# Kernel tuning notes

Measured on AMD Instinct MI355X. Metric: run time of the kernel, lower is better.

## Reference

```python
import jax, jax.numpy as jnp
import numpy as np

N_NODES = 100000


def gcn_conv(h, W, b, src, dst, n):
    # h: [N, Fin] -> [N, Fout], GCNConv with symmetric normalization + self-loops
    h = h @ W  # transform first (PyG order): [N, Fout]
    loop = jnp.arange(n, dtype=src.dtype)
    src_sl = jnp.concatenate([src, loop])  # [E+N]
    dst_sl = jnp.concatenate([dst, loop])
    deg = jax.ops.segment_sum(jnp.ones_like(dst_sl, dtype=h.dtype), dst_sl, num_segments=n)  # [N]
    dinv = jax.lax.rsqrt(deg)  # deg >= 1 thanks to self-loops
    norm = dinv[src_sl] * dinv[dst_sl]  # [E+N]
    msgs = h[src_sl] * norm[:, None]  # gather + scale: [E+N, Fout]
    out = jax.ops.segment_sum(msgs, dst_sl, num_segments=n)  # scatter-add
    return out + b


def setup_inputs() -> dict:
    key = jax.random.key(0)
    kx, ke, k1, k2 = jax.random.split(key, 4)
    in_dim, hid_dim, out_dim = 512, 128, 40
    x = jax.random.normal(kx, (N_NODES, in_dim), dtype=jnp.float32)
    edge_index = jax.random.randint(ke, (2, 1600000), 0, N_NODES, dtype=jnp.int64)
    s1 = 1.0 / np.sqrt(in_dim)
    s2 = 1.0 / np.sqrt(hid_dim)
    W1 = jax.random.uniform(k1, (in_dim, hid_dim), jnp.float32, -s1, s1)
    b1 = jnp.zeros((hid_dim,), jnp.float32)
    W2 = jax.random.uniform(k2, (hid_dim, out_dim), jnp.float32, -s2, s2)
    b2 = jnp.zeros((out_dim,), jnp.float32)
    return {"x": x, "edge_index": edge_index, "W1": W1, "b1": b1, "W2": W2, "b2": b2}


def reference(x, edge_index, W1, b1, W2, b2):
    src, dst = edge_index[0], edge_index[1]
    n = x.shape[0]
    h = jax.nn.relu(gcn_conv(x, W1, b1, src, dst, n))
    h = gcn_conv(h, W2, b2, src, dst, n)
    return jax.nn.log_softmax(h, axis=1)
```

## Files before the change

### kernel.cpp

```cpp
#include <hip/hip_runtime.h>
#include <math.h>

#define FIN 512
#define FH 128
#define FOUT 40
#define FP 64
#define NB 512
#define PSLOTS 30
#define CAPG 4096
#define PBLK 512

typedef unsigned char u8;
typedef __attribute__((ext_vector_type(8))) short bf16x8;
typedef __attribute__((ext_vector_type(4))) float f32x4;
typedef __attribute__((ext_vector_type(2))) float f32x2;

__device__ inline ushort f2bf(float f){
  union { float f; uint32_t u; } v; v.f = f;
  uint32_t u = v.u;
  uint32_t r = (u + 0x7FFF + ((u >> 16) & 1)) >> 16;
  return (ushort)r;
}
__device__ inline uint32_t cvtpk(float a, float b){
  uint32_t r;
  asm("v_cvt_pk_bf16_f32 %0, %1, %2" : "=v"(r) : "v"(a), "v"(b));
  return r;
}
__device__ inline f32x2 pkadd(f32x2 a, f32x2 b){
  f32x2 r;
  asm("v_pk_add_f32 %0, %1, %2" : "=v"(r) : "v"(a), "v"(b));
  return r;
}
__device__ inline f32x2 f8lo(uint32_t v){ return __builtin_amdgcn_cvt_pk_f32_fp8(v, false); }
__device__ inline f32x2 f8hi(uint32_t v){ return __builtin_amdgcn_cvt_pk_f32_fp8(v, true); }
__device__ inline u8 f2f8(float v){
  return (u8)(__builtin_amdgcn_cvt_pk_fp8_f32(v, v, 0, false) & 0xFF);
}

__global__ __launch_bounds__(256) void k_part(const int* __restrict__ src,
                                              const int* __restrict__ dst, int e,
                                              int* __restrict__ gcur,
                                              uint32_t* __restrict__ gbuf, int n, int npb,
                                              const float* __restrict__ W1,
                                              const float* __restrict__ W2,
                                              ushort* __restrict__ W1t, ushort* __restrict__ W2t){
  __shared__ uint32_t pbuf[NB*PSLOTS];
  __shared__ int lcnt[NB];
  int b = blockIdx.x, t = threadIdx.x;
  int gidx = b*256 + t;
  if(gidx < FIN*FH){
    int k = gidx / FH, c = gidx % FH;
    W1t[(size_t)c*FIN + k] = f2bf(W1[gidx]);
  }
  if(gidx < 48*FH){
    int c = gidx / FH, k = gidx % FH;
    W2t[gidx] = (c < FOUT) ? f2bf(W2[(size_t)k*FOUT + c]) : (ushort)0;
  }
  for(int i=t;i<NB;i+=256) lcnt[i]=0;
  __syncthreads();
  int chunk = (e + PBLK - 1) / PBLK;
  int base = b * chunk;
  int endE = base + chunk; if(endE > e) endE = e;
  if(base >= e) return;
  int rounds = (endE - base + 255) / 256;
  for(int rr=0; rr<rounds; ++rr){
    int i = base + rr*256 + t;
    if(i < endE){
      int s = src[i];
      int d = dst[i];
      int bk = d / npb;
      uint32_t pk_ = ((uint32_t)s << 8) | (uint32_t)(d - bk*npb);
      int slot = atomicAdd(&lcnt[bk], 1);
      if(slot < PSLOTS){
        pbuf[bk*PSLOTS + slot] = pk_;
      } else {
        int g = atomicAdd(&gcur[bk], 1);
        gbuf[(size_t)bk*CAPG + g] = pk_;
      }
    }
    __syncthreads();
    bool last = (rr == rounds-1);
    for(int tb=t; tb<NB; tb+=256){
      int c = lcnt[tb];
      int k = c < PSLOTS ? c : PSLOTS;
      if(k > 0 && (k >= 16 || last)){
        int g = atomicAdd(&gcur[tb], k);
        uint32_t* dstp = &gbuf[(size_t)tb*CAPG + g];
        const uint32_t* srcp = &pbuf[tb*PSLOTS];
        for(int q=0; q<k; q++) dstp[q] = srcp[q];
        lcnt[tb] = 0;
      }
    }
    __syncthreads();
  }
}

__global__ __launch_bounds__(512) void k_scan_g(const int* __restrict__ gcur,
                                                int* __restrict__ bstart){
  __shared__ int sh[512];
  int t = threadIdx.x;
  sh[t] = gcur[t];
  __syncthreads();
  for(int off=1; off<512; off<<=1){
    int x = (t>=off)? sh[t-off]:0; __syncthreads();
    sh[t]+=x; __syncthreads();
  }
  bstart[t] = (t>0)? sh[t-1] : 0;
}

__global__ __launch_bounds__(256) void k_histfill(const uint32_t* __restrict__ gbuf,
                                                  const int* __restrict__ gcur,
                                                  const int* __restrict__ bstart,
                                                  int* __restrict__ rp, float* __restrict__ dinv,
                                                  int* __restrict__ srcs, int n, int npb){
  __shared__ int hist[256];
  __shared__ int sh[256];
  __shared__ int lcur[256];
  int b = blockIdx.x, t = threadIdx.x;
  int base = b * npb;
  if(base >= n) return;
  int nn = n - base; if(nn > npb) nn = npb;
  hist[t] = 0;
  __syncthreads();
  int m = gcur[b];
  const uint32_t* bp = gbuf + (size_t)b*CAPG;
  for(int i=t; i<m; i+=256) atomicAdd(&hist[bp[i] & 255u], 1);
  __syncthreads();
  int v = hist[t];
  sh[t] = v;
  __syncthreads();
  for(int off=1; off<256; off<<=1){
    int x = (t>=off)? sh[t-off]:0; __syncthreads();
    sh[t]+=x; __syncthreads();
  }
  int bs = bstart[b];
  if(t < nn){
    rp[base+t+1] = bs + sh[t];
    dinv[base+t] = rsqrtf((float)(v+1));
    lcur[t] = bs + sh[t] - v;
  }
  if(b==0 && t==0) rp[0] = 0;
  __syncthreads();
  for(int i=t; i<m; i+=256){
    uint32_t w = bp[i];
    int ld = (int)(w & 255u);
    int p = atomicAdd(&lcur[ld], 1);
    srcs[p] = (int)(w >> 8);
  }
}

__global__ __launch_bounds__(512, 2) void k_gemm1(const float* __restrict__ X,
                                                  const ushort* __restrict__ W1t,
                                                  const float* __restrict__ dinv,
                                                  u8* __restrict__ XWs, int n){
  __shared__ char smem[32768];
  int t = threadIdx.x;
  int gi = blockIdx.x;
  int lane = t & 63;
  int wid = t >> 6;
  int l15 = lane & 15;
  int lk8 = (lane >> 4) * 8;
  int rowbase = gi * 256 + wid * 32;

  int r0 = rowbase + l15;      if (r0 >= n) r0 = n-1;
  int r1 = rowbase + 16 + l15; if (r1 >= n) r1 = n-1;
  const float* a0p = X + (size_t)r0*FIN;
  const float* a1p = X + (size_t)r1*FIN;

  f32x4 acc[2][8];
  #pragma unroll
  for(int i=0;i<2;i++)
    #pragma unroll
    for(int j=0;j<8;j++) acc[i][j] = (f32x4){0.f,0.f,0.f,0.f};

  char* WsB = smem;

  for(int ph=0; ph<4; ph++){
    if(ph) __syncthreads();
    #pragma unroll
    for(int it=0; it<4; it++){
      int c = it*512 + t;
      int col = c >> 4, kslot = c & 15;
      uint4 v = *(const uint4*)(W1t + (size_t)col*FIN + ph*128 + kslot*8);
      int dstb = col*256 + ((kslot*16) ^ ((col & 7) << 4));
      *(uint4*)(WsB + dstb) = v;
    }
    __syncthreads();

    for(int kc=0; kc<4; kc++){
      int kl = kc*32 + lk8;
      int kg = ph*128 + kl;
      float4 a0a = *(const float4*)(a0p + kg);
      float4 a0b = *(const float4*)(a0p + kg + 4);
      float4 a1a = *(const float4*)(a1p + kg);
      float4 a1b = *(const float4*)(a1p + kg + 4);
      uint4 fa0u, fa1u;
      fa0u.x = cvtpk(a0a.x, a0a.y); fa0u.y = cvtpk(a0a.z, a0a.w);
      fa0u.z = cvtpk(a0b.x, a0b.y); fa0u.w = cvtpk(a0b.z, a0b.w);
      fa1u.x = cvtpk(a1a.x, a1a.y); fa1u.y = cvtpk(a1a.z, a1a.w);
      fa1u.z = cvtpk(a1b.x, a1b.y); fa1u.w = cvtpk(a1b.z, a1b.w);
      bf16x8 fa0 = *(bf16x8*)&fa0u;
      bf16x8 fa1 = *(bf16x8*)&fa1u;

      #pragma unroll
      for(int fj=0; fj<8; fj++){
        int col = fj*16 + l15;
        int srcb = col*256 + ((kl*2) ^ ((col & 7) << 4));
        bf16x8 fb = *(const bf16x8*)(WsB + srcb);
        acc[0][fj] = __builtin_amdgcn_mfma_f32_16x16x32_bf16(fa0, fb, acc[0][fj], 0, 0, 0);
        acc[1][fj] = __builtin_amdgcn_mfma_f32_16x16x32_bf16(fa1, fb, acc[1][fj], 0, 0, 0);
      }
    }
  }

  int rbase = (lane >> 4) * 4;
  #pragma unroll
  for(int fi=0; fi<2; fi++){
    #pragma unroll
    for(int r=0; r<4; r++){
      int row = rowbase + fi*16 + rbase + r;
      if(row < n){
        float dd = dinv[row];
        #pragma unroll
        for(int fj=0; fj<8; fj++){
          XWs[(size_t)row*FH + fj*16 + l15] = f2f8(acc[fi][fj][r] * dd);
        }
      }
    }
  }
}

__global__ __launch_bounds__(256) void k_agg1(const u8* __restrict__ XWs, const int* __restrict__ rp,
                                              const int* __restrict__ srcs, const float* __restrict__ dinv,
                                              const float* __restrict__ b1, ushort* __restrict__ H1b, int n){
  int d = blockIdx.x*4 + (threadIdx.x >> 6);
  if(d >= n) return;
  int lane = threadIdx.x & 63;
  int g = lane >> 3, li = lane & 7;
  f32x2 acc[8];
  #pragma unroll
  for(int k=0;k<8;k++) acc[k] = (f32x2){0.f,0.f};
  int beg = rp[d];
  int end = rp[d+1];
  int j = beg + g;
  bool h0 = j < end, h1 = j + 8 < end;
  int s0 = 0, s1 = 0;
  if(h0) s0 = srcs[j];
  if(h1) s1 = srcs[j+8];
  while(h1){
    int nj = j + 16;
    bool nh0 = nj < end, nh1 = nj + 8 < end;
    int ns0 = 0, ns1 = 0;
    if(nh0) ns0 = srcs[nj];
    if(nh1) ns1 = srcs[nj+8];
    uint4 a0 = *(const uint4*)(XWs + (size_t)s0*FH + li*16);
    uint4 c0 = *(const uint4*)(XWs + (size_t)s1*FH + li*16);
    acc[0] = pkadd(acc[0], pkadd(f8lo(a0.x), f8lo(c0.x)));
    acc[1] = pkadd(acc[1], pkadd(f8hi(a0.x), f8hi(c0.x)));
    acc[2] = pkadd(acc[2], pkadd(f8lo(a0.y), f8lo(c0.y)));
    acc[3] = pkadd(acc[3], pkadd(f8hi(a0.y), f8hi(c0.y)));
    acc[4] = pkadd(acc[4], pkadd(f8lo(a0.z), f8lo(c0.z)));
    acc[5] = pkadd(acc[5], pkadd(f8hi(a0.z), f8hi(c0.z)));
    acc[6] = pkadd(acc[6], pkadd(f8lo(a0.w), f8lo(c0.w)));
    acc[7] = pkadd(acc[7], pkadd(f8hi(a0.w), f8hi(c0.w)));
    j = nj; s0 = ns0; s1 = ns1; h0 = nh0; h1 = nh1;
  }
  if(h0){
    uint4 a0 = *(const uint4*)(XWs + (size_t)s0*FH + li*16);
    acc[0] = pkadd(acc[0], f8lo(a0.x));
    acc[1] = pkadd(acc[1], f8hi(a0.x));
    acc[2] = pkadd(acc[2], f8lo(a0.y));
    acc[3] = pkadd(acc[3], f8hi(a0.y));
    acc[4] = pkadd(acc[4], f8lo(a0.z));
    acc[5] = pkadd(acc[5], f8hi(a0.z));
    acc[6] = pkadd(acc[6], f8lo(a0.w));
    acc[7] = pkadd(acc[7], f8hi(a0.w));
  }
  #pragma unroll
  for(int k=0;k<8;k++){
    #pragma unroll
    for(int c=0;c<2;c++){
      acc[k][c] += __shfl_xor(acc[k][c], 8);
      acc[k][c] += __shfl_xor(acc[k][c], 16);
      acc[k][c] += __shfl_xor(acc[k][c], 32);
    }
  }
  if(g == 0){
    uint4 sv4 = *(const uint4*)(XWs + (size_t)d*FH + li*16);
    f32x2 slf[8];
    slf[0]=f8lo(sv4.x); slf[1]=f8hi(sv4.x); slf[2]=f8lo(sv4.y); slf[3]=f8hi(sv4.y);
    slf[4]=f8lo(sv4.z); slf[5]=f8hi(sv4.z); slf[6]=f8lo(sv4.w); slf[7]=f8hi(sv4.w);
    float dd = dinv[d];
    uint32_t w[8];
    #pragma unroll
    for(int k=0;k<8;k++){
      float b0 = b1[li*16 + k*2];
      float b1v = b1[li*16 + k*2 + 1];
      float o0 = fmaxf((acc[k][0]+slf[k][0])*dd + b0, 0.f);
      float o1 = fmaxf((acc[k][1]+slf[k][1])*dd + b1v, 0.f);
      w[k] = cvtpk(o0, o1);
    }
    uint4 w0 = {w[0],w[1],w[2],w[3]};
    uint4 w1 = {w[4],w[5],w[6],w[7]};
    uint4* wp = (uint4*)(H1b + (size_t)d*FH + li*16);
    wp[0] = w0;
    wp[1] = w1;
  }
}

__global__ __launch_bounds__(256) void k_gemm2_mfma(const ushort* __restrict__ H1b,
                                                    const ushort* __restrict__ W2t,
                                                    const float* __restrict__ dinv,
                                                    u8* __restrict__ H2s, int n){
  int t = threadIdx.x;
  int lane = t & 63;
  int wid = t >> 6;
  int l15 = lane & 15;
  int lk8 = (lane >> 4) * 8;
  int rowbase = blockIdx.x * 128 + wid * 32;

  int r0 = rowbase + l15;      if (r0 >= n) r0 = n-1;
  int r1 = rowbase + 16 + l15; if (r1 >= n) r1 = n-1;
  const ushort* a0p = H1b + (size_t)r0*FH + lk8;
  const ushort* a1p = H1b + (size_t)r1*FH + lk8;

  f32x4 acc[2][3];
  #pragma unroll
  for(int i=0;i<2;i++)
    #pragma unroll
    for(int j=0;j<3;j++) acc[i][j] = (f32x4){0.f,0.f,0.f,0.f};

  #pragma unroll
  for(int kc=0; kc<4; kc++){
    int k0 = kc*32;
    bf16x8 fa0 = *(const bf16x8*)(a0p + k0);
    bf16x8 fa1 = *(const bf16x8*)(a1p + k0);
    #pragma unroll
    for(int fj=0; fj<3; fj++){
      bf16x8 fb = *(const bf16x8*)(W2t + (size_t)(fj*16 + l15)*FH + k0 + lk8);
      acc[0][fj] = __builtin_amdgcn_mfma_f32_16x16x32_bf16(fa0, fb, acc[0][fj], 0, 0, 0);
      acc[1][fj] = __builtin_amdgcn_mfma_f32_16x16x32_bf16(fa1, fb, acc[1][fj], 0, 0, 0);
    }
  }

  int rbase = (lane >> 4) * 4;
  #pragma unroll
  for(int fi=0; fi<2; fi++){
    #pragma unroll
    for(int r=0; r<4; r++){
      int row = rowbase + fi*16 + rbase + r;
      if(row < n){
        float dd = dinv[row];
        #pragma unroll
        for(int fj=0; fj<3; fj++){
          int col = fj*16 + l15;
          H2s[(size_t)row*FP + col] = (col < FOUT) ? f2f8(acc[fi][fj][r] * dd) : (u8)0;
        }
        H2s[(size_t)row*FP + 48 + l15] = (u8)0;
      }
    }
  }
}

__global__ __launch_bounds__(256) void k_agg2_sm(const u8* __restrict__ H2s, const int* __restrict__ rp,
                                                 const int* __restrict__ srcs, const float* __restrict__ dinv,
                                                 const float* __restrict__ b2, float* __restrict__ out, int n){
  int d = blockIdx.x*4 + (threadIdx.x >> 6);
  if(d >= n) return;
  int lane = threadIdx.x & 63;
  int g = lane >> 3, li = lane & 7;
  f32x2 acc[4];
  #pragma unroll
  for(int k=0;k<4;k++) acc[k] = (f32x2){0.f,0.f};
  int beg = rp[d];
  int end = rp[d+1];
  int j = beg + g;
  bool h0 = j < end, h1 = j + 8 < end;
  int s0 = 0, s1 = 0;
  if(h0) s0 = srcs[j];
  if(h1) s1 = srcs[j+8];
  while(h1){
    int nj = j + 16;
    bool nh0 = nj < end, nh1 = nj + 8 < end;
    int ns0 = 0, ns1 = 0;
    if(nh0) ns0 = srcs[nj];
    if(nh1) ns1 = srcs[nj+8];
    uint2 v = *(const uint2*)(H2s + (size_t)s0*FP + li*8);
    uint2 u = *(const uint2*)(H2s + (size_t)s1*FP + li*8);
    acc[0] = pkadd(acc[0], pkadd(f8lo(v.x), f8lo(u.x)));
    acc[1] = pkadd(acc[1], pkadd(f8hi(v.x), f8hi(u.x)));
    acc[2] = pkadd(acc[2], pkadd(f8lo(v.y), f8lo(u.y)));
    acc[3] = pkadd(acc[3], pkadd(f8hi(v.y), f8hi(u.y)));
    j = nj; s0 = ns0; s1 = ns1; h0 = nh0; h1 = nh1;
  }
  if(h0){
    uint2 v = *(const uint2*)(H2s + (size_t)s0*FP + li*8);
    acc[0] = pkadd(acc[0], f8lo(v.x));
    acc[1] = pkadd(acc[1], f8hi(v.x));
    acc[2] = pkadd(acc[2], f8lo(v.y));
    acc[3] = pkadd(acc[3], f8hi(v.y));
  }
  #pragma unroll
  for(int k=0;k<4;k++){
    #pragma unroll
    for(int c=0;c<2;c++){
      acc[k][c] += __shfl_xor(acc[k][c], 8);
      acc[k][c] += __shfl_xor(acc[k][c], 16);
      acc[k][c] += __shfl_xor(acc[k][c], 32);
    }
  }
  uint2 sv = *(const uint2*)(H2s + (size_t)d*FP + li*8);
  f32x2 s2[4] = { f8lo(sv.x), f8hi(sv.x), f8lo(sv.y), f8hi(sv.y) };
  float dd = dinv[d];
  float val[8];
  #pragma unroll
  for(int k=0;k<4;k++){
    #pragma unroll
    for(int c=0;c<2;c++){
      int col = li*8 + k*2 + c;
      float bv = (col < FOUT) ? b2[col] : 0.f;
      val[k*2+c] = (col < FOUT) ? ((acc[k][c]+s2[k][c])*dd + bv) : -3.402823466e38f;
    }
  }
  float m = val[0];
  #pragma unroll
  for(int k=1;k<8;k++) m = fmaxf(m, val[k]);
  #pragma unroll
  for(int off=1; off<8; off<<=1) m = fmaxf(m, __shfl_xor(m, off));
  float ssum = 0.f;
  #pragma unroll
  for(int k=0;k<8;k++){
    int col = li*8 + k;
    ssum += (col < FOUT) ? expf(val[k] - m) : 0.f;
  }
  #pragma unroll
  for(int off=1; off<8; off<<=1) ssum += __shfl_xor(ssum, off);
  float lse = m + logf(ssum);
  if(g == 0 && li < 5){
    float4 o0 = {val[0]-lse, val[1]-lse, val[2]-lse, val[3]-lse};
    float4 o1 = {val[4]-lse, val[5]-lse, val[6]-lse, val[7]-lse};
    float* op = out + (size_t)d*FOUT + li*8;
    *(float4*)op = o0;
    *(float4*)(op+4) = o1;
  }
}


extern "C" void kernel_launch(void* const* d_in, const int* in_sizes, int n_in,
                              void* d_out, int out_size, void* d_ws, size_t ws_size,
                              hipStream_t stream){
  const float* X  = (const float*)d_in[0];
  const int*   ei = (const int*)d_in[1];
  const float* W1 = (const float*)d_in[2];
  const float* b1 = (const float*)d_in[3];
  const float* W2 = (const float*)d_in[4];
  const float* b2 = (const float*)d_in[5];
  float* out = (float*)d_out;

  int n = in_sizes[0] / FIN;
  int e = in_sizes[1] / 2;
  const int* src = ei;
  const int* dst = ei + e;

  int npb = (n + NB - 1) / NB;

  u8* XWs     = (u8*)d_ws;
  ushort* H1b = (ushort*)(XWs + (size_t)n*FH);
  u8* H2s     = (u8*)(H1b + (size_t)n*FH);
  ushort* W1t = (ushort*)(H2s + (size_t)n*FP);
  ushort* W2t = W1t + (size_t)FH*FIN;
  float* dinv = (float*)(W2t + 48*FH);
  int* gcur   = (int*)(dinv + n);
  int* bstart = gcur + NB;
  int* rp     = bstart + NB;
  int* srcs   = rp + (n+1) + 3;
  uint32_t* gbuf = (uint32_t*)H1b;

  int G = (n + 255) / 256;

  hipMemsetAsync(gcur, 0, (size_t)NB*sizeof(int), stream);
  hipLaunchKernelGGL(k_part, dim3(PBLK), dim3(256), 0, stream,
                     src, dst, e, gcur, gbuf, n, npb, W1, W2, W1t, W2t);
  hipLaunchKernelGGL(k_scan_g, dim3(1), dim3(512), 0, stream, gcur, bstart);
  hipLaunchKernelGGL(k_histfill, dim3(NB), dim3(256), 0, stream,
                     gbuf, gcur, bstart, rp, dinv, srcs, n, npb);

  hipLaunchKernelGGL(k_gemm1, dim3(G), dim3(512), 0, stream, X, W1t, dinv, XWs, n);

  hipLaunchKernelGGL(k_agg1, dim3((n+3)/4), dim3(256), 0, stream, XWs, rp, srcs, dinv, b1, H1b, n);
  hipLaunchKernelGGL(k_gemm2_mfma, dim3((n+127)/128), dim3(256), 0, stream, H1b, W2t, dinv, H2s, n);
  hipLaunchKernelGGL(k_agg2_sm, dim3((n+3)/4), dim3(256), 0, stream, H2s, rp, srcs, dinv, b2, out, n);
}
```

Measured before the change: 239.1 us.

## Fuse edge partitioning with GEMM1 in one launch by interleaving block roles

Edge partitioning and the first GEMM now run in one kernel, with odd blocks doing the partition and even blocks doing the GEMM, so the memory-bound partition overlaps the MFMA work. Because the GEMM now runs before the degree/dinv computation, the source-side dinv scaling moves out of the GEMM epilogue into agg1, which gathers dinv[src] per edge and uses packed FMAs. Weight conversion is split into its own small prep kernel. The cost is one extra dinv gather per edge in the aggregation and higher shared-memory use per block, which may lower occupancy.

```diff
diff --git a/kernel.cpp b/kernel.cpp
--- a/kernel.cpp
+++ b/kernel.cpp
@@ -31,67 +31,159 @@
   asm("v_pk_add_f32 %0, %1, %2" : "=v"(r) : "v"(a), "v"(b));
   return r;
 }
+__device__ inline f32x2 pkfma(f32x2 a, f32x2 b, f32x2 c){
+  f32x2 r;
+  asm("v_pk_fma_f32 %0, %1, %2, %3" : "=v"(r) : "v"(a), "v"(b), "v"(c));
+  return r;
+}
 __device__ inline f32x2 f8lo(uint32_t v){ return __builtin_amdgcn_cvt_pk_f32_fp8(v, false); }
 __device__ inline f32x2 f8hi(uint32_t v){ return __builtin_amdgcn_cvt_pk_f32_fp8(v, true); }
 __device__ inline u8 f2f8(float v){
   return (u8)(__builtin_amdgcn_cvt_pk_fp8_f32(v, v, 0, false) & 0xFF);
 }
 
-__global__ __launch_bounds__(256) void k_part(const int* __restrict__ src,
-                                              const int* __restrict__ dst, int e,
-                                              int* __restrict__ gcur,
-                                              uint32_t* __restrict__ gbuf, int n, int npb,
-                                              const float* __restrict__ W1,
+__global__ __launch_bounds__(256) void k_prep(const float* __restrict__ W1,
                                               const float* __restrict__ W2,
                                               ushort* __restrict__ W1t, ushort* __restrict__ W2t){
-  __shared__ uint32_t pbuf[NB*PSLOTS];
-  __shared__ int lcnt[NB];
-  int b = blockIdx.x, t = threadIdx.x;
-  int gidx = b*256 + t;
-  if(gidx < FIN*FH){
-    int k = gidx / FH, c = gidx % FH;
-    W1t[(size_t)c*FIN + k] = f2bf(W1[gidx]);
-  }
-  if(gidx < 48*FH){
-    int c = gidx / FH, k = gidx % FH;
-    W2t[gidx] = (c < FOUT) ? f2bf(W2[(size_t)k*FOUT + c]) : (ushort)0;
-  }
-  for(int i=t;i<NB;i+=256) lcnt[i]=0;
-  __syncthreads();
-  int chunk = (e + PBLK - 1) / PBLK;
-  int base = b * chunk;
-  int endE = base + chunk; if(endE > e) endE = e;
-  if(base >= e) return;
-  int rounds = (endE - base + 255) / 256;
-  for(int rr=0; rr<rounds; ++rr){
-    int i = base + rr*256 + t;
-    if(i < endE){
-      int s = src[i];
-      int d = dst[i];
-      int bk = d / npb;
-      uint32_t pk_ = ((uint32_t)s << 8) | (uint32_t)(d - bk*npb);
-      int slot = atomicAdd(&lcnt[bk], 1);
-      if(slot < PSLOTS){
-        pbuf[bk*PSLOTS + slot] = pk_;
-      } else {
-        int g = atomicAdd(&gcur[bk], 1);
-        gbuf[(size_t)bk*CAPG + g] = pk_;
+  int i = blockIdx.x*256 + threadIdx.x;
+  if(i < FIN*FH){
+    int k = i / FH, c = i % FH;
+    W1t[(size_t)c*FIN + k] = f2bf(W1[i]);
+  }
+  if(i < 48*FH){
+    int c = i / FH, k = i % FH;
+    W2t[i] = (c < FOUT) ? f2bf(W2[(size_t)k*FOUT + c]) : (ushort)0;
+  }
+}
+
+__global__ __launch_bounds__(512, 2) void k_gemm1_part(const float* __restrict__ X,
+                                                       const ushort* __restrict__ W1t,
+                                                       u8* __restrict__ XWs, int n, int G,
+                                                       const int* __restrict__ src,
+                                                       const int* __restrict__ dst, int e,
+                                                       int* __restrict__ gcur,
+                                                       uint32_t* __restrict__ gbuf, int npb){
+  __shared__ char smem[63488];
+  int b = blockIdx.x;
+  int t = threadIdx.x;
+
+  if(b & 1){
+    int pidx = b >> 1;
+    if(pidx >= PBLK) return;
+    uint32_t* pbuf = (uint32_t*)smem;
+    int* lcnt = (int*)(smem + NB*PSLOTS*4);
+    if(t < NB) lcnt[t] = 0;
+    __syncthreads();
+    int chunk = (e + PBLK - 1) / PBLK;
+    int base = pidx * chunk;
+    int endE = base + chunk; if(endE > e) endE = e;
+    if(base >= e) return;
+    int rounds = (endE - base + 511) / 512;
+    for(int rr=0; rr<rounds; ++rr){
+      int i = base + rr*512 + t;
+      if(i < endE){
+        int s = src[i];
+        int d = dst[i];
+        int bk = d / npb;
+        uint32_t pk_ = ((uint32_t)s << 8) | (uint32_t)(d - bk*npb);
+        int slot = atomicAdd(&lcnt[bk], 1);
+        if(slot < PSLOTS){
+          pbuf[bk*PSLOTS + slot] = pk_;
+        } else {
+          int g = atomicAdd(&gcur[bk], 1);
+          gbuf[(size_t)bk*CAPG + g] = pk_;
+        }
       }
+      __syncthreads();
+      bool last = (rr == rounds-1);
+      if(t < NB){
+        int c = lcnt[t];
+        int k = c < PSLOTS ? c : PSLOTS;
+        if(k > 0 && (k >= 16 || last)){
+          int g = atomicAdd(&gcur[t], k);
+          uint32_t* dstp = &gbuf[(size_t)t*CAPG + g];
+          const uint32_t* srcp = &pbuf[t*PSLOTS];
+          for(int q=0; q<k; q++) dstp[q] = srcp[q];
+          lcnt[t] = 0;
+        }
+      }
+      __syncthreads();
+    }
+    return;
+  }
+
+  int gi = b >> 1;
+  if(gi >= G) return;
+  int lane = t & 63;
+  int wid = t >> 6;
+  int l15 = lane & 15;
+  int lk8 = (lane >> 4) * 8;
+  int rowbase = gi * 256 + wid * 32;
+
+  int r0 = rowbase + l15;      if (r0 >= n) r0 = n-1;
+  int r1 = rowbase + 16 + l15; if (r1 >= n) r1 = n-1;
+  const float* a0p = X + (size_t)r0*FIN;
+  const float* a1p = X + (size_t)r1*FIN;
+
+  f32x4 acc[2][8];
+  #pragma unroll
+  for(int i=0;i<2;i++)
+    #pragma unroll
+    for(int j=0;j<8;j++) acc[i][j] = (f32x4){0.f,0.f,0.f,0.f};
+
+  char* WsB = smem;
+
+  for(int ph=0; ph<4; ph++){
+    if(ph) __syncthreads();
+    #pragma unroll
+    for(int it=0; it<4; it++){
+      int c = it*512 + t;
+      int col = c >> 4, kslot = c & 15;
+      uint4 v = *(const uint4*)(W1t + (size_t)col*FIN + ph*128 + kslot*8);
+      int dstb = col*256 + ((kslot*16) ^ ((col & 7) << 4));
+      *(uint4*)(WsB + dstb) = v;
     }
     __syncthreads();
-    bool last = (rr == rounds-1);
-    for(int tb=t; tb<NB; tb+=256){
-      int c = lcnt[tb];
-      int k = c < PSLOTS ? c : PSLOTS;
-      if(k > 0 && (k >= 16 || last)){
-        int g = atomicAdd(&gcur[tb], k);
-        uint32_t* dstp = &gbuf[(size_t)tb*CAPG + g];
-        const uint32_t* srcp = &pbuf[tb*PSLOTS];
-        for(int q=0; q<k; q++) dstp[q] = srcp[q];
-        lcnt[tb] = 0;
+
+    for(int kc=0; kc<4; kc++){
+      int kl = kc*32 + lk8;
+      int kg = ph*128 + kl;
+      float4 a0a = *(const float4*)(a0p + kg);
+      float4 a0b = *(const float4*)(a0p + kg + 4);
+      float4 a1a = *(const float4*)(a1p + kg);
+      float4 a1b = *(const float4*)(a1p + kg + 4);
+      uint4 fa0u, fa1u;
+      fa0u.x = cvtpk(a0a.x, a0a.y); fa0u.y = cvtpk(a0a.z, a0a.w);
+      fa0u.z = cvtpk(a0b.x, a0b.y); fa0u.w = cvtpk(a0b.z, a0b.w);
+      fa1u.x = cvtpk(a1a.x, a1a.y); fa1u.y = cvtpk(a1a.z, a1a.w);
+      fa1u.z = cvtpk(a1b.x, a1b.y); fa1u.w = cvtpk(a1b.z, a1b.w);
+      bf16x8 fa0 = *(bf16x8*)&fa0u;
+      bf16x8 fa1 = *(bf16x8*)&fa1u;
+
+      #pragma unroll
+      for(int fj=0; fj<8; fj++){
+        int col = fj*16 + l15;
+        int srcb = col*256 + ((kl*2) ^ ((col & 7) << 4));
+        bf16x8 fb = *(const bf16x8*)(WsB + srcb);
+        acc[0][fj] = __builtin_amdgcn_mfma_f32_16x16x32_bf16(fa0, fb, acc[0][fj], 0, 0, 0);
+        acc[1][fj] = __builtin_amdgcn_mfma_f32_16x16x32_bf16(fa1, fb, acc[1][fj], 0, 0, 0);
       }
     }
-    __syncthreads();
+  }
+
+  int rbase = (lane >> 4) * 4;
+  #pragma unroll
+  for(int fi=0; fi<2; fi++){
+    #pragma unroll
+    for(int r=0; r<4; r++){
+      int row = rowbase + fi*16 + rbase + r;
+      if(row < n){
+        #pragma unroll
+        for(int fj=0; fj<8; fj++){
+          XWs[(size_t)row*FH + fj*16 + l15] = f2f8(acc[fi][fj][r]);
+        }
+      }
+    }
   }
 }
 
@@ -149,87 +241,6 @@
   }
 }
 
-__global__ __launch_bounds__(512, 2) void k_gemm1(const float* __restrict__ X,
-                                                  const ushort* __restrict__ W1t,
-                                                  const float* __restrict__ dinv,
-                                                  u8* __restrict__ XWs, int n){
-  __shared__ char smem[32768];
-  int t = threadIdx.x;
-  int gi = blockIdx.x;
-  int lane = t & 63;
-  int wid = t >> 6;
-  int l15 = lane & 15;
-  int lk8 = (lane >> 4) * 8;
-  int rowbase = gi * 256 + wid * 32;
-
-  int r0 = rowbase + l15;      if (r0 >= n) r0 = n-1;
-  int r1 = rowbase + 16 + l15; if (r1 >= n) r1 = n-1;
-  const float* a0p = X + (size_t)r0*FIN;
-  const float* a1p = X + (size_t)r1*FIN;
-
-  f32x4 acc[2][8];
-  #pragma unroll
-  for(int i=0;i<2;i++)
-    #pragma unroll
-    for(int j=0;j<8;j++) acc[i][j] = (f32x4){0.f,0.f,0.f,0.f};
-
-  char* WsB = smem;
-
-  for(int ph=0; ph<4; ph++){
-    if(ph) __syncthreads();
-    #pragma unroll
-    for(int it=0; it<4; it++){
-      int c = it*512 + t;
-      int col = c >> 4, kslot = c & 15;
-      uint4 v = *(const uint4*)(W1t + (size_t)col*FIN + ph*128 + kslot*8);
-      int dstb = col*256 + ((kslot*16) ^ ((col & 7) << 4));
-      *(uint4*)(WsB + dstb) = v;
-    }
-    __syncthreads();
-
-    for(int kc=0; kc<4; kc++){
-      int kl = kc*32 + lk8;
-      int kg = ph*128 + kl;
-      float4 a0a = *(const float4*)(a0p + kg);
-      float4 a0b = *(const float4*)(a0p + kg + 4);
-      float4 a1a = *(const float4*)(a1p + kg);
-      float4 a1b = *(const float4*)(a1p + kg + 4);
-      uint4 fa0u, fa1u;
-      fa0u.x = cvtpk(a0a.x, a0a.y); fa0u.y = cvtpk(a0a.z, a0a.w);
-      fa0u.z = cvtpk(a0b.x, a0b.y); fa0u.w = cvtpk(a0b.z, a0b.w);
-      fa1u.x = cvtpk(a1a.x, a1a.y); fa1u.y = cvtpk(a1a.z, a1a.w);
-      fa1u.z = cvtpk(a1b.x, a1b.y); fa1u.w = cvtpk(a1b.z, a1b.w);
-      bf16x8 fa0 = *(bf16x8*)&fa0u;
-      bf16x8 fa1 = *(bf16x8*)&fa1u;
-
-      #pragma unroll
-      for(int fj=0; fj<8; fj++){
-        int col = fj*16 + l15;
-        int srcb = col*256 + ((kl*2) ^ ((col & 7) << 4));
-        bf16x8 fb = *(const bf16x8*)(WsB + srcb);
-        acc[0][fj] = __builtin_amdgcn_mfma_f32_16x16x32_bf16(fa0, fb, acc[0][fj], 0, 0, 0);
-        acc[1][fj] = __builtin_amdgcn_mfma_f32_16x16x32_bf16(fa1, fb, acc[1][fj], 0, 0, 0);
-      }
-    }
-  }
-
-  int rbase = (lane >> 4) * 4;
-  #pragma unroll
-  for(int fi=0; fi<2; fi++){
-    #pragma unroll
-    for(int r=0; r<4; r++){
-      int row = rowbase + fi*16 + rbase + r;
-      if(row < n){
-        float dd = dinv[row];
-        #pragma unroll
-        for(int fj=0; fj<8; fj++){
-          XWs[(size_t)row*FH + fj*16 + l15] = f2f8(acc[fi][fj][r] * dd);
-        }
-      }
-    }
-  }
-}
-
 __global__ __launch_bounds__(256) void k_agg1(const u8* __restrict__ XWs, const int* __restrict__ rp,
                                               const int* __restrict__ srcs, const float* __restrict__ dinv,
                                               const float* __restrict__ b1, ushort* __restrict__ H1b, int n){
@@ -245,36 +256,41 @@
   int j = beg + g;
   bool h0 = j < end, h1 = j + 8 < end;
   int s0 = 0, s1 = 0;
-  if(h0) s0 = srcs[j];
-  if(h1) s1 = srcs[j+8];
+  float ds0 = 0.f, ds1 = 0.f;
+  if(h0){ s0 = srcs[j];   ds0 = dinv[s0]; }
+  if(h1){ s1 = srcs[j+8]; ds1 = dinv[s1]; }
   while(h1){
     int nj = j + 16;
     bool nh0 = nj < end, nh1 = nj + 8 < end;
     int ns0 = 0, ns1 = 0;
-    if(nh0) ns0 = srcs[nj];
-    if(nh1) ns1 = srcs[nj+8];
+    float nds0 = 0.f, nds1 = 0.f;
+    if(nh0){ ns0 = srcs[nj];   nds0 = dinv[ns0]; }
+    if(nh1){ ns1 = srcs[nj+8]; nds1 = dinv[ns1]; }
     uint4 a0 = *(const uint4*)(XWs + (size_t)s0*FH + li*16);
     uint4 c0 = *(const uint4*)(XWs + (size_t)s1*FH + li*16);
-    acc[0] = pkadd(acc[0], pkadd(f8lo(a0.x), f8lo(c0.x)));
-    acc[1] = pkadd(acc[1], pkadd(f8hi(a0.x), f8hi(c0.x)));
-    acc[2] = pkadd(acc[2], pkadd(f8lo(a0.y), f8lo(c0.y)));
-    acc[3] = pkadd(acc[3], pkadd(f8hi(a0.y), f8hi(c0.y)));
-    acc[4] = pkadd(acc[4], pkadd(f8lo(a0.z), f8lo(c0.z)));
-    acc[5] = pkadd(acc[5], pkadd(f8hi(a0.z), f8hi(c0.z)));
-    acc[6] = pkadd(acc[6], pkadd(f8lo(a0.w), f8lo(c0.w)));
-    acc[7] = pkadd(acc[7], pkadd(f8hi(a0.w), f8hi(c0.w)));
-    j = nj; s0 = ns0; s1 = ns1; h0 = nh0; h1 = nh1;
+    f32x2 d0v = {ds0, ds0};
+    f32x2 d1v = {ds1, ds1};
+    acc[0] = pkfma(f8lo(a0.x), d0v, acc[0]); acc[0] = pkfma(f8lo(c0.x), d1v, acc[0]);
+    acc[1] = pkfma(f8hi(a0.x), d0v, acc[1]); acc[1] = pkfma(f8hi(c0.x), d1v, acc[1]);
+    acc[2] = pkfma(f8lo(a0.y), d0v, acc[2]); acc[2] = pkfma(f8lo(c0.y), d1v, acc[2]);
+    acc[3] = pkfma(f8hi(a0.y), d0v, acc[3]); acc[3] = pkfma(f8hi(c0.y), d1v, acc[3]);
+    acc[4] = pkfma(f8lo(a0.z), d0v, acc[4]); acc[4] = pkfma(f8lo(c0.z), d1v, acc[4]);
+    acc[5] = pkfma(f8hi(a0.z), d0v, acc[5]); acc[5] = pkfma(f8hi(c0.z), d1v, acc[5]);
+    acc[6] = pkfma(f8lo(a0.w), d0v, acc[6]); acc[6] = pkfma(f8lo(c0.w), d1v, acc[6]);
+    acc[7] = pkfma(f8hi(a0.w), d0v, acc[7]); acc[7] = pkfma(f8hi(c0.w), d1v, acc[7]);
+    j = nj; s0 = ns0; s1 = ns1; ds0 = nds0; ds1 = nds1; h0 = nh0; h1 = nh1;
   }
   if(h0){
     uint4 a0 = *(const uint4*)(XWs + (size_t)s0*FH + li*16);
-    acc[0] = pkadd(acc[0], f8lo(a0.x));
-    acc[1] = pkadd(acc[1], f8hi(a0.x));
-    acc[2] = pkadd(acc[2], f8lo(a0.y));
-    acc[3] = pkadd(acc[3], f8hi(a0.y));
-    acc[4] = pkadd(acc[4], f8lo(a0.z));
-    acc[5] = pkadd(acc[5], f8hi(a0.z));
-    acc[6] = pkadd(acc[6], f8lo(a0.w));
-    acc[7] = pkadd(acc[7], f8hi(a0.w));
+    f32x2 d0v = {ds0, ds0};
+    acc[0] = pkfma(f8lo(a0.x), d0v, acc[0]);
+    acc[1] = pkfma(f8hi(a0.x), d0v, acc[1]);
+    acc[2] = pkfma(f8lo(a0.y), d0v, acc[2]);
+    acc[3] = pkfma(f8hi(a0.y), d0v, acc[3]);
+    acc[4] = pkfma(f8lo(a0.z), d0v, acc[4]);
+    acc[5] = pkfma(f8hi(a0.z), d0v, acc[5]);
+    acc[6] = pkfma(f8lo(a0.w), d0v, acc[6]);
+    acc[7] = pkfma(f8hi(a0.w), d0v, acc[7]);
   }
   #pragma unroll
   for(int k=0;k<8;k++){
@@ -296,8 +312,8 @@
     for(int k=0;k<8;k++){
       float b0 = b1[li*16 + k*2];
       float b1v = b1[li*16 + k*2 + 1];
-      float o0 = fmaxf((acc[k][0]+slf[k][0])*dd + b0, 0.f);
-      float o1 = fmaxf((acc[k][1]+slf[k][1])*dd + b1v, 0.f);
+      float o0 = fmaxf((acc[k][0] + slf[k][0]*dd)*dd + b0, 0.f);
+      float o1 = fmaxf((acc[k][1] + slf[k][1]*dd)*dd + b1v, 0.f);
       w[k] = cvtpk(o0, o1);
     }
     uint4 w0 = {w[0],w[1],w[2],w[3]};
@@ -477,16 +493,16 @@
   uint32_t* gbuf = (uint32_t*)H1b;
 
   int G = (n + 255) / 256;
+  int T = 2 * ((G > PBLK) ? G : PBLK);
 
   hipMemsetAsync(gcur, 0, (size_t)NB*sizeof(int), stream);
-  hipLaunchKernelGGL(k_part, dim3(PBLK), dim3(256), 0, stream,
-                     src, dst, e, gcur, gbuf, n, npb, W1, W2, W1t, W2t);
+  hipLaunchKernelGGL(k_prep, dim3((FIN*FH+255)/256), dim3(256), 0, stream, W1, W2, W1t, W2t);
+  hipLaunchKernelGGL(k_gemm1_part, dim3(T), dim3(512), 0, stream,
+                     X, W1t, XWs, n, G, src, dst, e, gcur, gbuf, npb);
   hipLaunchKernelGGL(k_scan_g, dim3(1), dim3(512), 0, stream, gcur, bstart);
   hipLaunchKernelGGL(k_histfill, dim3(NB), dim3(256), 0, stream,
                      gbuf, gcur, bstart, rp, dinv, srcs, n, npb);
 
-  hipLaunchKernelGGL(k_gemm1, dim3(G), dim3(512), 0, stream, X, W1t, dinv, XWs, n);
-
   hipLaunchKernelGGL(k_agg1, dim3((n+3)/4), dim3(256), 0, stream, XWs, rp, srcs, dinv, b1, H1b, n);
   hipLaunchKernelGGL(k_gemm2_mfma, dim3((n+127)/128), dim3(256), 0, stream, H1b, W2t, dinv, H2s, n);
   hipLaunchKernelGGL(k_agg2_sm, dim3((n+3)/4), dim3(256), 0, stream, H2s, rp, srcs, dinv, b2, out, n);
```

After: 252.5 us. 5.6% more time.
